# Optimization experiments

Hardware: AMD Instinct MI355X
Metric: run time of the kernel (lower is better)

The kernel has to match this reference:

```python
import jax, jax.numpy as jnp
import numpy as np

B, S, H = 2, 1024, 1024
NH, NKV, HD = 16, 4, 64
E, K, I = 8, 2, 3584
EPS = 1e-5
THETA = 1e6


def setup_inputs() -> dict:
    key = jax.random.key(0)
    ks = jax.random.split(key, 12)
    sc = 0.02
    return {
        "hidden_states": jax.random.normal(ks[0], (B, S, H), jnp.float32),
        "ln1_w": jnp.ones((H,), jnp.float32),
        "wq": jax.random.normal(ks[1], (H, NH * HD), jnp.float32) * sc,
        "wk": jax.random.normal(ks[2], (H, NKV * HD), jnp.float32) * sc,
        "wv": jax.random.normal(ks[3], (H, NKV * HD), jnp.float32) * sc,
        "wo": jax.random.normal(ks[4], (NH * HD, H), jnp.float32) * sc,
        "ln2_w": jnp.ones((H,), jnp.float32),
        "router_w": jax.random.normal(ks[5], (H, E), jnp.float32) * sc,
        "w_gate": jax.random.normal(ks[6], (E, H, I), jnp.float32) * sc,
        "w_up": jax.random.normal(ks[7], (E, H, I), jnp.float32) * sc,
        "w_down": jax.random.normal(ks[8], (E, I, H), jnp.float32) * sc,
    }


def _rmsnorm(x, w):
    xf = x.astype(jnp.float32)
    return (xf * jax.lax.rsqrt(jnp.mean(xf * xf, axis=-1, keepdims=True) + EPS)).astype(x.dtype) * w


def _rope_cos_sin():
    inv_freq = 1.0 / (THETA ** (jnp.arange(0, HD, 2, dtype=jnp.float32) / HD))
    ang = jnp.arange(S, dtype=jnp.float32)[:, None] * inv_freq[None, :]  # [S, HD//2]
    emb = jnp.concatenate([ang, ang], axis=-1)  # [S, HD]
    return jnp.cos(emb)[None, :, None, :], jnp.sin(emb)[None, :, None, :]


def _rotate_half(x):
    return jnp.concatenate([-x[..., HD // 2:], x[..., : HD // 2]], axis=-1)


def _attention(x, wq, wk, wv, wo):
    q = (x @ wq).reshape(B, S, NH, HD)
    k = (x @ wk).reshape(B, S, NKV, HD)
    v = (x @ wv).reshape(B, S, NKV, HD)
    cos, sin = _rope_cos_sin()
    q = q * cos + _rotate_half(q) * sin
    k = k * cos + _rotate_half(k) * sin
    rep = NH // NKV
    k = jnp.repeat(k, rep, axis=2)  # [B,S,NH,HD]
    v = jnp.repeat(v, rep, axis=2)
    scores = jnp.einsum("bqhd,bkhd->bhqk", q, k) / jnp.sqrt(jnp.float32(HD))
    causal = jnp.tril(jnp.ones((S, S), bool))
    scores = jnp.where(causal[None, None], scores, jnp.float32(-1e9))
    probs = jax.nn.softmax(scores, axis=-1)
    out = jnp.einsum("bhqk,bkhd->bqhd", probs, v).reshape(B, S, NH * HD)
    return out @ wo


def _moe(x, router_w, w_gate, w_up, w_down):
    t = x.reshape(B * S, H)  # [T,H]
    logits = t @ router_w  # [T,E]
    probs = jax.nn.softmax(logits.astype(jnp.float32), axis=-1)
    top_v, top_i = jax.lax.top_k(probs, K)
    top_v = top_v / jnp.sum(top_v, axis=-1, keepdims=True)  # normalize_top_k_affinities
    # dense combine weights [T,E]
    dense_w = jnp.sum(jax.nn.one_hot(top_i, E, dtype=t.dtype) * top_v[..., None], axis=1)
    out = jnp.zeros_like(t)
    for e in range(E):  # small fixed expert loop (E=8)
        g = jax.nn.silu(t @ w_gate[e]) * (t @ w_up[e])
        out = out + dense_w[:, e:e + 1] * (g @ w_down[e])
    return out.reshape(B, S, H)


def reference(hidden_states, ln1_w, wq, wk, wv, wo, ln2_w, router_w, w_gate, w_up, w_down):
    residual = hidden_states
    h = _rmsnorm(hidden_states, ln1_w)
    h = residual + _attention(h, wq, wk, wv, wo)
    residual = h
    h2 = _rmsnorm(h, ln2_w)
    h = residual + _moe(h2, router_w, w_gate, w_up, w_down)
    return h
```

## Files before the change

### kernel.cpp

```cpp
#include <hip/hip_runtime.h>
#include <hip/hip_bf16.h>
#include <math.h>

#define B_ 2
#define S_ 1024
#define H_ 1024
#define NH_ 16
#define NKV_ 4
#define HD_ 64
#define E_ 8
#define I_ 3584
#define T_ (B_*S_)

#define BM 64
#define BN 64
#define BK 32
#define MBM 128
#define MBK 64

typedef __bf16 bf16x8 __attribute__((ext_vector_type(8)));
typedef float f32x4 __attribute__((ext_vector_type(4)));

__device__ __forceinline__ __bf16 bf_hi(float f) { return (__bf16)f; }
__device__ __forceinline__ __bf16 bf_lo(float f, __bf16 h) { return (__bf16)(f - (float)h); }

__device__ __forceinline__ int swz(int row, int col) {
    return (row * 64 + col * 2) ^ (((row >> 3) & 7) << 4);
}
__device__ __forceinline__ int swz128(int row, int col) {
    return (row * 128 + col * 2) ^ ((row & 7) << 4);
}

__global__ __launch_bounds__(256) void cvt_bf16_kernel(
    const float* __restrict__ src, __bf16* __restrict__ dst, int n8)
{
    int idx = blockIdx.x * 256 + threadIdx.x;
    if (idx >= n8) return;
    const float4* s = (const float4*)src + (size_t)idx * 2;
    float4 a = s[0], b = s[1];
    bf16x8 v;
    v[0] = (__bf16)a.x; v[1] = (__bf16)a.y; v[2] = (__bf16)a.z; v[3] = (__bf16)a.w;
    v[4] = (__bf16)b.x; v[5] = (__bf16)b.y; v[6] = (__bf16)b.z; v[7] = (__bf16)b.w;
    ((bf16x8*)dst)[idx] = v;
}

__global__ __launch_bounds__(256) void transpose_cvt_kernel(
    const float* __restrict__ src, __bf16* __restrict__ dst, int M, int N)
{
    int e = blockIdx.z;
    src += (size_t)e * M * N;
    dst += (size_t)e * M * N;
    int n0 = blockIdx.x * 64, m0 = blockIdx.y * 64;
    __shared__ __bf16 Ts[64][72];
    int tid = threadIdx.x;
#pragma unroll
    for (int i = 0; i < 16; i++) {
        int row = i * 4 + (tid >> 6);
        int col = tid & 63;
        Ts[row][col] = (__bf16)src[(size_t)(m0 + row) * N + n0 + col];
    }
    __syncthreads();
#pragma unroll
    for (int j = 0; j < 2; j++) {
        int n = (tid >> 3) + j * 32;
        int k8 = (tid & 7) * 8;
        bf16x8 v;
#pragma unroll
        for (int ii = 0; ii < 8; ii++) v[ii] = Ts[k8 + ii][n];
        *(bf16x8*)(dst + (size_t)(n0 + n) * M + m0 + k8) = v;
    }
}

__global__ __launch_bounds__(256) void rmsnorm_kernel(
    const float* __restrict__ x, const float* __restrict__ w, float* __restrict__ out)
{
    int row = blockIdx.x;
    int tid = threadIdx.x;
    const float* xr = x + (size_t)row * H_;
    float vals[4];
    float ss = 0.f;
#pragma unroll
    for (int i = 0; i < 4; i++) {
        vals[i] = xr[tid + 256 * i];
        ss += vals[i] * vals[i];
    }
#pragma unroll
    for (int off = 32; off; off >>= 1) ss += __shfl_xor(ss, off);
    __shared__ float red[4];
    int wid = tid >> 6;
    if ((tid & 63) == 0) red[wid] = ss;
    __syncthreads();
    float tot = red[0] + red[1] + red[2] + red[3];
    float scale = rsqrtf(tot * (1.0f / H_) + 1e-5f);
#pragma unroll
    for (int i = 0; i < 4; i++)
        out[(size_t)row * H_ + tid + 256 * i] = vals[i] * scale * w[tid + 256 * i];
}

__global__ __launch_bounds__(256) void gemm_bf16(
    const float* __restrict__ A, const float* __restrict__ Bm,
    float* __restrict__ C, const float* __restrict__ res,
    int M, int N, int Kd)
{
    __shared__ __bf16 As[BM * BK];
    __shared__ __bf16 Bs[BN * BK];
    char* Asb = (char*)As;
    char* Bsb = (char*)Bs;
    int tid = threadIdx.x;
    int lane = tid & 63, wid = tid >> 6;
    int wm = wid >> 1, wn = wid & 1;
    int m0 = blockIdx.y * BM, n0 = blockIdx.x * BN;
    f32x4 acc[2][2] = {};
    int ar = tid >> 2, ac = (tid & 3) * 8;
    int bk = tid >> 3, bc = (tid & 7) * 8;
    for (int kt = 0; kt < Kd; kt += BK) {
        const float* ag = A + (size_t)(m0 + ar) * Kd + kt + ac;
        bf16x8 av;
#pragma unroll
        for (int i = 0; i < 8; i++) av[i] = (__bf16)ag[i];
        *(bf16x8*)(Asb + swz(ar, ac)) = av;
        const float* bg = Bm + (size_t)(kt + bk) * N + n0 + bc;
#pragma unroll
        for (int i = 0; i < 8; i++)
            *(__bf16*)(Bsb + swz(bc + i, bk)) = (__bf16)bg[i];
        __syncthreads();
        int r = lane & 15, k8 = (lane >> 4) * 8;
        bf16x8 af[2], bfr[2];
#pragma unroll
        for (int m = 0; m < 2; m++) af[m] = *(const bf16x8*)(Asb + swz(wm * 32 + m * 16 + r, k8));
#pragma unroll
        for (int n = 0; n < 2; n++) bfr[n] = *(const bf16x8*)(Bsb + swz(wn * 32 + n * 16 + r, k8));
#pragma unroll
        for (int m = 0; m < 2; m++)
#pragma unroll
            for (int n = 0; n < 2; n++)
                acc[m][n] = __builtin_amdgcn_mfma_f32_16x16x32_bf16(af[m], bfr[n], acc[m][n], 0, 0, 0);
        __syncthreads();
    }
    int cl = lane & 15, rb = (lane >> 4) * 4;
#pragma unroll
    for (int m = 0; m < 2; m++)
#pragma unroll
        for (int n = 0; n < 2; n++)
#pragma unroll
            for (int j = 0; j < 4; j++) {
                int row = m0 + wm * 32 + m * 16 + rb + j;
                int col = n0 + wn * 32 + n * 16 + cl;
                size_t o = (size_t)row * N + col;
                float v = acc[m][n][j];
                if (res) v += res[o];
                C[o] = v;
            }
}

__global__ void rope_kernel(float* __restrict__ x, int heads, int total)
{
    int idx = blockIdx.x * blockDim.x + threadIdx.x;
    if (idx >= total) return;
    int j = idx & 31;
    int th = idx >> 5;
    int h = th % heads;
    int t = th / heads;
    int s = t & (S_ - 1);
    float inv = powf(1e6f, -(float)j / 32.0f);
    float ang = (float)s * inv;
    float c = cosf(ang), sn = sinf(ang);
    size_t base = (size_t)t * heads * HD_ + (size_t)h * HD_;
    float x1 = x[base + j], x2 = x[base + 32 + j];
    x[base + j] = x1 * c - x2 * sn;
    x[base + 32 + j] = x2 * c + x1 * sn;
}

#define LP 72
__global__ __launch_bounds__(256) void flash_kernel(
    const float* __restrict__ q, const float* __restrict__ k,
    const float* __restrict__ v, float* __restrict__ o)
{
    __shared__ __bf16 Ks [64][LP];
    __shared__ __bf16 Ksl[64][LP];
    __shared__ __bf16 Vt [64][LP];
    __shared__ __bf16 Vtl[64][LP];
    __shared__ __bf16 Pl [4][16][LP];
    __shared__ __bf16 Pll[4][16][LP];

    int tid = threadIdx.x;
    int lane = tid & 63, wid = tid >> 6;
    int qr = lane & 15, quad = lane >> 4;
    int qt = (S_ / 16 - 1) - blockIdx.x;
    int kvh = blockIdx.y, b = blockIdx.z;
    int h = kvh * 4 + wid;
    int s0 = qt * 16;

    const float* qg = q + ((size_t)(b * S_ + s0 + qr) * NH_ + h) * HD_ + quad * 8;
    bf16x8 qf[2], qlo[2];
#pragma unroll
    for (int ks = 0; ks < 2; ks++)
#pragma unroll
        for (int i = 0; i < 8; i++) {
            float f = qg[ks * 32 + i] * 0.125f;
            __bf16 hh = bf_hi(f);
            qf[ks][i] = hh;
            qlo[ks][i] = bf_lo(f, hh);
        }

    float m_run[4], l_run[4];
    f32x4 o_acc[4] = {};
#pragma unroll
    for (int j = 0; j < 4; j++) { m_run[j] = -1e30f; l_run[j] = 0.f; }

    int skey = tid >> 2, shd0 = (tid & 3) * 16;
    int vhd = tid & 63, vkey0 = (tid >> 6) * 16;

    for (int kt = 0; kt <= s0 + 15; kt += 64) {
        __syncthreads();
        {
            const float* kg = k + ((size_t)(b * S_ + kt + skey) * NKV_ + kvh) * HD_ + shd0;
#pragma unroll
            for (int i = 0; i < 16; i++) {
                float f = kg[i];
                __bf16 hh = bf_hi(f);
                Ks [skey][shd0 + i] = hh;
                Ksl[skey][shd0 + i] = bf_lo(f, hh);
            }
        }
        {
            const float* vg = v + ((size_t)(b * S_ + kt + vkey0) * NKV_ + kvh) * HD_ + vhd;
#pragma unroll
            for (int i = 0; i < 16; i++) {
                float val = vg[(size_t)i * (NKV_ * HD_)];
                __bf16 hh = bf_hi(val);
                Vt [vhd][vkey0 + i] = hh;
                Vtl[vhd][vkey0 + i] = bf_lo(val, hh);
            }
        }
        __syncthreads();

        f32x4 sc4[4];
#pragma unroll
        for (int sub = 0; sub < 4; sub++) {
            int krow = sub * 16 + qr;
            bf16x8 kh0 = *(const bf16x8*)&Ks [krow][quad * 8];
            bf16x8 kh1 = *(const bf16x8*)&Ks [krow][32 + quad * 8];
            bf16x8 kl0 = *(const bf16x8*)&Ksl[krow][quad * 8];
            bf16x8 kl1 = *(const bf16x8*)&Ksl[krow][32 + quad * 8];
            f32x4 z = {};
            z = __builtin_amdgcn_mfma_f32_16x16x32_bf16(qf[0],  kh0, z, 0, 0, 0);
            z = __builtin_amdgcn_mfma_f32_16x16x32_bf16(qf[1],  kh1, z, 0, 0, 0);
            z = __builtin_amdgcn_mfma_f32_16x16x32_bf16(qlo[0], kh0, z, 0, 0, 0);
            z = __builtin_amdgcn_mfma_f32_16x16x32_bf16(qlo[1], kh1, z, 0, 0, 0);
            z = __builtin_amdgcn_mfma_f32_16x16x32_bf16(qf[0],  kl0, z, 0, 0, 0);
            z = __builtin_amdgcn_mfma_f32_16x16x32_bf16(qf[1],  kl1, z, 0, 0, 0);
            sc4[sub] = z;
        }
        if (kt + 63 > s0) {
#pragma unroll
            for (int sub = 0; sub < 4; sub++)
#pragma unroll
                for (int j = 0; j < 4; j++) {
                    int key = kt + sub * 16 + qr;
                    int row = s0 + quad * 4 + j;
                    if (key > row) sc4[sub][j] = -1e30f;
                }
        }
#pragma unroll
        for (int j = 0; j < 4; j++) {
            float mx = fmaxf(fmaxf(sc4[0][j], sc4[1][j]), fmaxf(sc4[2][j], sc4[3][j]));
#pragma unroll
            for (int off = 1; off < 16; off <<= 1) mx = fmaxf(mx, __shfl_xor(mx, off));
            float mn = fmaxf(m_run[j], mx);
            float scale = __expf(m_run[j] - mn);
            m_run[j] = mn;
            float rs = 0.f;
#pragma unroll
            for (int sub = 0; sub < 4; sub++) {
                float pe = __expf(sc4[sub][j] - mn);
                sc4[sub][j] = pe;
                rs += pe;
            }
#pragma unroll
            for (int off = 1; off < 16; off <<= 1) rs += __shfl_xor(rs, off);
            l_run[j] = l_run[j] * scale + rs;
#pragma unroll
            for (int sub = 0; sub < 4; sub++) o_acc[sub][j] *= scale;
        }
#pragma unroll
        for (int sub = 0; sub < 4; sub++)
#pragma unroll
            for (int j = 0; j < 4; j++) {
                float pe = sc4[sub][j];
                __bf16 hh = bf_hi(pe);
                Pl [wid][quad * 4 + j][sub * 16 + qr] = hh;
                Pll[wid][quad * 4 + j][sub * 16 + qr] = bf_lo(pe, hh);
            }
        __syncthreads();
        bf16x8 ph0 = *(const bf16x8*)&Pl [wid][qr][quad * 8];
        bf16x8 ph1 = *(const bf16x8*)&Pl [wid][qr][32 + quad * 8];
        bf16x8 pl0 = *(const bf16x8*)&Pll[wid][qr][quad * 8];
        bf16x8 pl1 = *(const bf16x8*)&Pll[wid][qr][32 + quad * 8];
#pragma unroll
        for (int sub = 0; sub < 4; sub++) {
            int vrow = sub * 16 + qr;
            bf16x8 vh0 = *(const bf16x8*)&Vt [vrow][quad * 8];
            bf16x8 vh1 = *(const bf16x8*)&Vt [vrow][32 + quad * 8];
            bf16x8 vl0 = *(const bf16x8*)&Vtl[vrow][quad * 8];
            bf16x8 vl1 = *(const bf16x8*)&Vtl[vrow][32 + quad * 8];
            o_acc[sub] = __builtin_amdgcn_mfma_f32_16x16x32_bf16(ph0, vh0, o_acc[sub], 0, 0, 0);
            o_acc[sub] = __builtin_amdgcn_mfma_f32_16x16x32_bf16(ph1, vh1, o_acc[sub], 0, 0, 0);
            o_acc[sub] = __builtin_amdgcn_mfma_f32_16x16x32_bf16(ph0, vl0, o_acc[sub], 0, 0, 0);
            o_acc[sub] = __builtin_amdgcn_mfma_f32_16x16x32_bf16(ph1, vl1, o_acc[sub], 0, 0, 0);
            o_acc[sub] = __builtin_amdgcn_mfma_f32_16x16x32_bf16(pl0, vh0, o_acc[sub], 0, 0, 0);
            o_acc[sub] = __builtin_amdgcn_mfma_f32_16x16x32_bf16(pl1, vh1, o_acc[sub], 0, 0, 0);
        }
    }
#pragma unroll
    for (int j = 0; j < 4; j++) {
        float inv = 1.f / l_run[j];
        int row = s0 + quad * 4 + j;
#pragma unroll
        for (int sub = 0; sub < 4; sub++)
            o[((size_t)(b * S_ + row) * NH_ + h) * HD_ + sub * 16 + qr] = o_acc[sub][j] * inv;
    }
}

__global__ __launch_bounds__(256) void router_kernel(
    const float* __restrict__ xn, const float* __restrict__ rw,
    int* __restrict__ top_i, float* __restrict__ top_w)
{
    int wid = threadIdx.x >> 6, lane = threadIdx.x & 63;
    int t = blockIdx.x * 4 + wid;
    const float* xr = xn + (size_t)t * H_;
    float acc[E_] = {};
    for (int c = 0; c < H_ / 64; c++) {
        float xd = xr[c * 64 + lane];
        const float* wrow = rw + (size_t)(c * 64 + lane) * E_;
#pragma unroll
        for (int e = 0; e < E_; e++) acc[e] += xd * wrow[e];
    }
#pragma unroll
    for (int e = 0; e < E_; e++) {
        float r = acc[e];
#pragma unroll
        for (int off = 32; off; off >>= 1) r += __shfl_xor(r, off);
        acc[e] = r;
    }
    if (lane == 0) {
        float mx = acc[0];
        for (int e = 1; e < E_; e++) mx = fmaxf(mx, acc[e]);
        float p[E_], sum = 0.f;
        for (int e = 0; e < E_; e++) { p[e] = __expf(acc[e] - mx); sum += p[e]; }
        float inv_s = 1.f / sum;
        for (int e = 0; e < E_; e++) p[e] *= inv_s;
        int i0 = 0;
        for (int e = 1; e < E_; e++) if (p[e] > p[i0]) i0 = e;
        int i1 = (i0 == 0) ? 1 : 0;
        for (int e = 0; e < E_; e++) if (e != i0 && p[e] > p[i1]) i1 = e;
        float v0 = p[i0], v1 = p[i1], inv = 1.f / (v0 + v1);
        top_i[t * 2] = i0; top_i[t * 2 + 1] = i1;
        top_w[t * 2] = v0 * inv; top_w[t * 2 + 1] = v1 * inv;
    }
}

__global__ void assign_kernel(
    const int* __restrict__ top_i, const float* __restrict__ top_w,
    int* __restrict__ tlist, int* __restrict__ pair_pos,
    int* __restrict__ counts, int* __restrict__ offsets)
{
    __shared__ int cnt[E_], off[E_], fill[E_];
    int tid = threadIdx.x;
    if (tid < E_) { cnt[tid] = 0; fill[tid] = 0; }
    __syncthreads();
    for (int t = tid; t < T_; t += 256) {
        atomicAdd(&cnt[top_i[t * 2]], 1);
        atomicAdd(&cnt[top_i[t * 2 + 1]], 1);
    }
    __syncthreads();
    if (tid == 0) {
        int o = 0;
        for (int e = 0; e < E_; e++) { off[e] = o; o += cnt[e]; }
    }
    __syncthreads();
    for (int t = tid; t < T_; t += 256) {
        for (int j = 0; j < 2; j++) {
            int e = top_i[t * 2 + j];
            int pos = off[e] + atomicAdd(&fill[e], 1);
            tlist[pos] = t;
            pair_pos[t * 2 + j] = pos;
        }
    }
    __syncthreads();
    if (tid < E_) { counts[tid] = cnt[tid]; offsets[tid] = off[tid]; }
}

__global__ __launch_bounds__(256) void moe_gemm_gateup(
    const __bf16* __restrict__ Xb, const __bf16* __restrict__ WgT, const __bf16* __restrict__ WuT,
    __bf16* __restrict__ act, const int* __restrict__ tlist,
    const int* __restrict__ counts, const int* __restrict__ offsets)
{
    int e = blockIdx.z;
    int cnt = counts[e], off = offsets[e];
    int m0 = blockIdx.y * MBM;
    if (m0 >= cnt) return;
    int n0 = blockIdx.x * BN;
    const __bf16* Bg = WgT + (size_t)e * H_ * I_;
    const __bf16* Bu = WuT + (size_t)e * H_ * I_;
    __shared__ __bf16 As[MBM * MBK];
    __shared__ __bf16 Gs[BN * MBK];
    __shared__ __bf16 Us[BN * MBK];
    __shared__ int rowidx[MBM];
    char* Asb = (char*)As;
    char* Gsb = (char*)Gs;
    char* Usb = (char*)Us;
    int tid = threadIdx.x;
    if (tid < MBM) {
        int rl = m0 + tid;
        rowidx[tid] = tlist[off + ((rl < cnt) ? rl : 0)];
    }
    __syncthreads();
    int lane = tid & 63, wid = tid >> 6;
    f32x4 accg[2][4] = {}, accu[2][4] = {};
    int ar = tid >> 1, ac = (tid & 1) * 32;
    int bn = tid >> 2, bc = (tid & 3) * 16;
    const __bf16* abase = Xb + (size_t)rowidx[ar] * H_;
    for (int kt = 0; kt < H_; kt += MBK) {
#pragma unroll
        for (int g = 0; g < 4; g++)
            *(bf16x8*)(Asb + swz128(ar, ac + g * 8)) =
                *(const bf16x8*)(abase + kt + ac + g * 8);
        const __bf16* gr = Bg + (size_t)(n0 + bn) * H_ + kt + bc;
        const __bf16* ur = Bu + (size_t)(n0 + bn) * H_ + kt + bc;
#pragma unroll
        for (int g = 0; g < 2; g++) {
            *(bf16x8*)(Gsb + swz128(bn, bc + g * 8)) = *(const bf16x8*)(gr + g * 8);
            *(bf16x8*)(Usb + swz128(bn, bc + g * 8)) = *(const bf16x8*)(ur + g * 8);
        }
        __syncthreads();
        int r = lane & 15, q8 = (lane >> 4) * 8;
#pragma unroll
        for (int kk = 0; kk < 2; kk++) {
            bf16x8 af[2], gf[4], uf[4];
#pragma unroll
            for (int m = 0; m < 2; m++)
                af[m] = *(const bf16x8*)(Asb + swz128(wid * 32 + m * 16 + r, kk * 32 + q8));
#pragma unroll
            for (int n = 0; n < 4; n++) {
                gf[n] = *(const bf16x8*)(Gsb + swz128(n * 16 + r, kk * 32 + q8));
                uf[n] = *(const bf16x8*)(Usb + swz128(n * 16 + r, kk * 32 + q8));
            }
#pragma unroll
            for (int m = 0; m < 2; m++)
#pragma unroll
                for (int n = 0; n < 4; n++) {
                    accg[m][n] = __builtin_amdgcn_mfma_f32_16x16x32_bf16(af[m], gf[n], accg[m][n], 0, 0, 0);
                    accu[m][n] = __builtin_amdgcn_mfma_f32_16x16x32_bf16(af[m], uf[n], accu[m][n], 0, 0, 0);
                }
        }
        __syncthreads();
    }
    int cl = lane & 15, rb = (lane >> 4) * 4;
#pragma unroll
    for (int m = 0; m < 2; m++)
#pragma unroll
        for (int n = 0; n < 4; n++)
#pragma unroll
            for (int j = 0; j < 4; j++) {
                int rl = m0 + wid * 32 + m * 16 + rb + j;
                if (rl >= cnt) continue;
                int col = n0 + n * 16 + cl;
                float g = accg[m][n][j], u = accu[m][n][j];
                float sig = 1.f / (1.f + __expf(-g));
                act[(size_t)(off + rl) * I_ + col] = (__bf16)(g * sig * u);
            }
}

__global__ __launch_bounds__(256) void moe_gemm_down(
    const __bf16* __restrict__ act, const __bf16* __restrict__ WdT,
    float* __restrict__ dout, const int* __restrict__ counts, const int* __restrict__ offsets)
{
    int e = blockIdx.z;
    int cnt = counts[e], off = offsets[e];
    int m0 = blockIdx.y * MBM;
    if (m0 >= cnt) return;
    int n0 = blockIdx.x * BN;
    const __bf16* Bw = WdT + (size_t)e * I_ * H_;
    __shared__ __bf16 As[MBM * MBK];
    __shared__ __bf16 Bs[BN * MBK];
    char* Asb = (char*)As;
    char* Bsb = (char*)Bs;
    int tid = threadIdx.x;
    int lane = tid & 63, wid = tid >> 6;
    f32x4 acc[2][4] = {};
    int ar = tid >> 1, ac = (tid & 1) * 32;
    int bn = tid >> 2, bc = (tid & 3) * 16;
    int arow = m0 + ar; if (arow >= cnt) arow = cnt - 1;
    const __bf16* abase = act + (size_t)(off + arow) * I_;
    for (int kt = 0; kt < I_; kt += MBK) {
#pragma unroll
        for (int g = 0; g < 4; g++)
            *(bf16x8*)(Asb + swz128(ar, ac + g * 8)) =
                *(const bf16x8*)(abase + kt + ac + g * 8);
        const __bf16* br = Bw + (size_t)(n0 + bn) * I_ + kt + bc;
#pragma unroll
        for (int g = 0; g < 2; g++)
            *(bf16x8*)(Bsb + swz128(bn, bc + g * 8)) = *(const bf16x8*)(br + g * 8);
        __syncthreads();
        int r = lane & 15, q8 = (lane >> 4) * 8;
#pragma unroll
        for (int kk = 0; kk < 2; kk++) {
            bf16x8 af[2], bfr[4];
#pragma unroll
            for (int m = 0; m < 2; m++)
                af[m] = *(const bf16x8*)(Asb + swz128(wid * 32 + m * 16 + r, kk * 32 + q8));
#pragma unroll
            for (int n = 0; n < 4; n++)
                bfr[n] = *(const bf16x8*)(Bsb + swz128(n * 16 + r, kk * 32 + q8));
#pragma unroll
            for (int m = 0; m < 2; m++)
#pragma unroll
                for (int n = 0; n < 4; n++)
                    acc[m][n] = __builtin_amdgcn_mfma_f32_16x16x32_bf16(af[m], bfr[n], acc[m][n], 0, 0, 0);
        }
        __syncthreads();
    }
    int cl = lane & 15, rb = (lane >> 4) * 4;
#pragma unroll
    for (int m = 0; m < 2; m++)
#pragma unroll
        for (int n = 0; n < 4; n++)
#pragma unroll
            for (int j = 0; j < 4; j++) {
                int rl = m0 + wid * 32 + m * 16 + rb + j;
                if (rl >= cnt) continue;
                int col = n0 + n * 16 + cl;
                dout[(size_t)(off + rl) * H_ + col] = acc[m][n][j];
            }
}

__global__ __launch_bounds__(256) void combine_kernel(
    const float* __restrict__ hres, const float* __restrict__ dout,
    const int* __restrict__ pair_pos, const float* __restrict__ top_w,
    float* __restrict__ out)
{
    int idx = blockIdx.x * 256 + threadIdx.x;
    int t = idx >> 10, d = idx & 1023;
    float v = hres[idx];
    int p0 = pair_pos[t * 2], p1 = pair_pos[t * 2 + 1];
    v += top_w[t * 2] * dout[(size_t)p0 * H_ + d]
       + top_w[t * 2 + 1] * dout[(size_t)p1 * H_ + d];
    out[idx] = v;
}

extern "C" void kernel_launch(void* const* d_in, const int* in_sizes, int n_in,
                              void* d_out, int out_size, void* d_ws, size_t ws_size,
                              hipStream_t stream) {
    const float* hidden = (const float*)d_in[0];
    const float* ln1 = (const float*)d_in[1];
    const float* wq = (const float*)d_in[2];
    const float* wk = (const float*)d_in[3];
    const float* wv = (const float*)d_in[4];
    const float* wo = (const float*)d_in[5];
    const float* ln2 = (const float*)d_in[6];
    const float* rw = (const float*)d_in[7];
    const float* wg = (const float*)d_in[8];
    const float* wu = (const float*)d_in[9];
    const float* wd = (const float*)d_in[10];
    float* out = (float*)d_out;

    char* ws = (char*)d_ws;
    size_t o = 0;
    auto alloc = [&](size_t bytes) -> void* {
        void* p = ws + o;
        o += (bytes + 255) & ~(size_t)255;
        return p;
    };
    float* xn   = (float*)alloc((size_t)T_ * H_ * 4);
    float* qb   = (float*)alloc((size_t)T_ * NH_ * HD_ * 4);
    float* kb   = (float*)alloc((size_t)T_ * NKV_ * HD_ * 4);
    float* vb   = (float*)alloc((size_t)T_ * NKV_ * HD_ * 4);
    float* attn = (float*)alloc((size_t)T_ * H_ * 4);
    float* hres = (float*)alloc((size_t)T_ * H_ * 4);
    int*   top_i    = (int*)alloc((size_t)T_ * 2 * 4);
    float* top_w    = (float*)alloc((size_t)T_ * 2 * 4);
    int*   pair_pos = (int*)alloc((size_t)T_ * 2 * 4);
    int*   tlist    = (int*)alloc((size_t)T_ * 2 * 4);
    int*   counts   = (int*)alloc(E_ * 4);
    int*   offsets  = (int*)alloc(E_ * 4);
    __bf16* actb  = (__bf16*)alloc((size_t)T_ * 2 * I_ * 2);
    float*  doutb = (float*)alloc((size_t)T_ * 2 * H_ * 4);
    __bf16* xnb = (__bf16*)alloc((size_t)T_ * H_ * 2);
    __bf16* wgt = (__bf16*)alloc((size_t)E_ * H_ * I_ * 2);
    __bf16* wut = (__bf16*)alloc((size_t)E_ * H_ * I_ * 2);
    __bf16* wdt = (__bf16*)alloc((size_t)E_ * I_ * H_ * 2);

    transpose_cvt_kernel<<<dim3(I_ / 64, H_ / 64, E_), 256, 0, stream>>>(wg, wgt, H_, I_);
    transpose_cvt_kernel<<<dim3(I_ / 64, H_ / 64, E_), 256, 0, stream>>>(wu, wut, H_, I_);
    transpose_cvt_kernel<<<dim3(H_ / 64, I_ / 64, E_), 256, 0, stream>>>(wd, wdt, I_, H_);

    rmsnorm_kernel<<<T_, 256, 0, stream>>>(hidden, ln1, xn);
    gemm_bf16<<<dim3((NH_ * HD_) / BN, T_ / BM), 256, 0, stream>>>(xn, wq, qb, nullptr, T_, NH_ * HD_, H_);
    gemm_bf16<<<dim3((NKV_ * HD_) / BN, T_ / BM), 256, 0, stream>>>(xn, wk, kb, nullptr, T_, NKV_ * HD_, H_);
    gemm_bf16<<<dim3((NKV_ * HD_) / BN, T_ / BM), 256, 0, stream>>>(xn, wv, vb, nullptr, T_, NKV_ * HD_, H_);
    {
        int tq = T_ * NH_ * 32, tk = T_ * NKV_ * 32;
        rope_kernel<<<(tq + 255) / 256, 256, 0, stream>>>(qb, NH_, tq);
        rope_kernel<<<(tk + 255) / 256, 256, 0, stream>>>(kb, NKV_, tk);
    }
    flash_kernel<<<dim3(S_ / 16, NKV_, B_), 256, 0, stream>>>(qb, kb, vb, attn);
    gemm_bf16<<<dim3(H_ / BN, T_ / BM), 256, 0, stream>>>(attn, wo, hres, hidden, T_, H_, H_);
    rmsnorm_kernel<<<T_, 256, 0, stream>>>(hres, ln2, xn);
    cvt_bf16_kernel<<<(T_ * H_ / 8 + 255) / 256, 256, 0, stream>>>(xn, xnb, T_ * H_ / 8);
    router_kernel<<<T_ / 4, 256, 0, stream>>>(xn, rw, top_i, top_w);
    assign_kernel<<<1, 256, 0, stream>>>(top_i, top_w, tlist, pair_pos, counts, offsets);
    moe_gemm_gateup<<<dim3(I_ / BN, T_ / MBM, E_), 256, 0, stream>>>(xnb, wgt, wut, actb, tlist, counts, offsets);
    moe_gemm_down<<<dim3(H_ / BN, T_ / MBM, E_), 256, 0, stream>>>(actb, wdt, doutb, counts, offsets);
    combine_kernel<<<(T_ * H_) / 256, 256, 0, stream>>>(hres, doutb, pair_pos, top_w, out);
}
```

Before: 524.4 us.

## Prefetch next K-tile into registers in MoE GEMMs and shrink down-proj M tile

Both MoE GEMM kernels now load the next K-tile from global memory into registers while MFMAs run on the current shared-memory tile, so load latency can overlap with compute. The down-projection also drops its M tile from 128 to 64 rows, doubling the grid so more workgroups are available for the roughly 512 assigned tokens per expert. This costs extra registers for the prefetch buffers and reuses each weight tile across fewer rows in the down GEMM.

```diff
diff --git a/kernel.cpp b/kernel.cpp
--- a/kernel.cpp
+++ b/kernel.cpp
@@ -16,6 +16,7 @@
 #define BN 64
 #define BK 32
 #define MBM 128
+#define DBM 64
 #define MBK 64
 
 typedef __bf16 bf16x8 __attribute__((ext_vector_type(8)));
@@ -420,20 +421,36 @@
     f32x4 accg[2][4] = {}, accu[2][4] = {};
     int ar = tid >> 1, ac = (tid & 1) * 32;
     int bn = tid >> 2, bc = (tid & 3) * 16;
-    const __bf16* abase = Xb + (size_t)rowidx[ar] * H_;
+    const __bf16* abase = Xb + (size_t)rowidx[ar] * H_ + ac;
+    const __bf16* gbase = Bg + (size_t)(n0 + bn) * H_ + bc;
+    const __bf16* ubase = Bu + (size_t)(n0 + bn) * H_ + bc;
+    bf16x8 pa[4], pg[2], pu[2];
+#pragma unroll
+    for (int g = 0; g < 4; g++) pa[g] = *(const bf16x8*)(abase + g * 8);
+#pragma unroll
+    for (int g = 0; g < 2; g++) {
+        pg[g] = *(const bf16x8*)(gbase + g * 8);
+        pu[g] = *(const bf16x8*)(ubase + g * 8);
+    }
     for (int kt = 0; kt < H_; kt += MBK) {
 #pragma unroll
-        for (int g = 0; g < 4; g++)
-            *(bf16x8*)(Asb + swz128(ar, ac + g * 8)) =
-                *(const bf16x8*)(abase + kt + ac + g * 8);
-        const __bf16* gr = Bg + (size_t)(n0 + bn) * H_ + kt + bc;
-        const __bf16* ur = Bu + (size_t)(n0 + bn) * H_ + kt + bc;
+        for (int g = 0; g < 4; g++) *(bf16x8*)(Asb + swz128(ar, ac + g * 8)) = pa[g];
 #pragma unroll
         for (int g = 0; g < 2; g++) {
-            *(bf16x8*)(Gsb + swz128(bn, bc + g * 8)) = *(const bf16x8*)(gr + g * 8);
-            *(bf16x8*)(Usb + swz128(bn, bc + g * 8)) = *(const bf16x8*)(ur + g * 8);
-        }
-        __syncthreads();
+            *(bf16x8*)(Gsb + swz128(bn, bc + g * 8)) = pg[g];
+            *(bf16x8*)(Usb + swz128(bn, bc + g * 8)) = pu[g];
+        }
+        __syncthreads();
+        int kn = kt + MBK;
+        if (kn < H_) {
+#pragma unroll
+            for (int g = 0; g < 4; g++) pa[g] = *(const bf16x8*)(abase + kn + g * 8);
+#pragma unroll
+            for (int g = 0; g < 2; g++) {
+                pg[g] = *(const bf16x8*)(gbase + kn + g * 8);
+                pu[g] = *(const bf16x8*)(ubase + kn + g * 8);
+            }
+        }
         int r = lane & 15, q8 = (lane >> 4) * 8;
 #pragma unroll
         for (int kk = 0; kk < 2; kk++) {
@@ -478,61 +495,67 @@
 {
     int e = blockIdx.z;
     int cnt = counts[e], off = offsets[e];
-    int m0 = blockIdx.y * MBM;
+    int m0 = blockIdx.y * DBM;
     if (m0 >= cnt) return;
     int n0 = blockIdx.x * BN;
     const __bf16* Bw = WdT + (size_t)e * I_ * H_;
-    __shared__ __bf16 As[MBM * MBK];
+    __shared__ __bf16 As[DBM * MBK];
     __shared__ __bf16 Bs[BN * MBK];
     char* Asb = (char*)As;
     char* Bsb = (char*)Bs;
     int tid = threadIdx.x;
     int lane = tid & 63, wid = tid >> 6;
-    f32x4 acc[2][4] = {};
-    int ar = tid >> 1, ac = (tid & 1) * 32;
+    f32x4 acc[4] = {};
+    int ar = tid >> 2, ac = (tid & 3) * 16;
     int bn = tid >> 2, bc = (tid & 3) * 16;
     int arow = m0 + ar; if (arow >= cnt) arow = cnt - 1;
-    const __bf16* abase = act + (size_t)(off + arow) * I_;
+    const __bf16* abase = act + (size_t)(off + arow) * I_ + ac;
+    const __bf16* bbase = Bw + (size_t)(n0 + bn) * I_ + bc;
+    bf16x8 pa[2], pb[2];
+#pragma unroll
+    for (int g = 0; g < 2; g++) {
+        pa[g] = *(const bf16x8*)(abase + g * 8);
+        pb[g] = *(const bf16x8*)(bbase + g * 8);
+    }
     for (int kt = 0; kt < I_; kt += MBK) {
 #pragma unroll
-        for (int g = 0; g < 4; g++)
-            *(bf16x8*)(Asb + swz128(ar, ac + g * 8)) =
-                *(const bf16x8*)(abase + kt + ac + g * 8);
-        const __bf16* br = Bw + (size_t)(n0 + bn) * I_ + kt + bc;
-#pragma unroll
-        for (int g = 0; g < 2; g++)
-            *(bf16x8*)(Bsb + swz128(bn, bc + g * 8)) = *(const bf16x8*)(br + g * 8);
-        __syncthreads();
+        for (int g = 0; g < 2; g++) {
+            *(bf16x8*)(Asb + swz128(ar, ac + g * 8)) = pa[g];
+            *(bf16x8*)(Bsb + swz128(bn, bc + g * 8)) = pb[g];
+        }
+        __syncthreads();
+        int kn = kt + MBK;
+        if (kn < I_) {
+#pragma unroll
+            for (int g = 0; g < 2; g++) {
+                pa[g] = *(const bf16x8*)(abase + kn + g * 8);
+                pb[g] = *(const bf16x8*)(bbase + kn + g * 8);
+            }
+        }
         int r = lane & 15, q8 = (lane >> 4) * 8;
 #pragma unroll
         for (int kk = 0; kk < 2; kk++) {
-            bf16x8 af[2], bfr[4];
-#pragma unroll
-            for (int m = 0; m < 2; m++)
-                af[m] = *(const bf16x8*)(Asb + swz128(wid * 32 + m * 16 + r, kk * 32 + q8));
+            bf16x8 af = *(const bf16x8*)(Asb + swz128(wid * 16 + r, kk * 32 + q8));
+            bf16x8 bfr[4];
 #pragma unroll
             for (int n = 0; n < 4; n++)
                 bfr[n] = *(const bf16x8*)(Bsb + swz128(n * 16 + r, kk * 32 + q8));
 #pragma unroll
-            for (int m = 0; m < 2; m++)
-#pragma unroll
-                for (int n = 0; n < 4; n++)
-                    acc[m][n] = __builtin_amdgcn_mfma_f32_16x16x32_bf16(af[m], bfr[n], acc[m][n], 0, 0, 0);
+            for (int n = 0; n < 4; n++)
+                acc[n] = __builtin_amdgcn_mfma_f32_16x16x32_bf16(af, bfr[n], acc[n], 0, 0, 0);
         }
         __syncthreads();
     }
     int cl = lane & 15, rb = (lane >> 4) * 4;
 #pragma unroll
-    for (int m = 0; m < 2; m++)
-#pragma unroll
-        for (int n = 0; n < 4; n++)
-#pragma unroll
-            for (int j = 0; j < 4; j++) {
-                int rl = m0 + wid * 32 + m * 16 + rb + j;
-                if (rl >= cnt) continue;
-                int col = n0 + n * 16 + cl;
-                dout[(size_t)(off + rl) * H_ + col] = acc[m][n][j];
-            }
+    for (int n = 0; n < 4; n++)
+#pragma unroll
+        for (int j = 0; j < 4; j++) {
+            int rl = m0 + wid * 16 + rb + j;
+            if (rl >= cnt) continue;
+            int col = n0 + n * 16 + cl;
+            dout[(size_t)(off + rl) * H_ + col] = acc[n][j];
+        }
 }
 
 __global__ __launch_bounds__(256) void combine_kernel(
@@ -611,6 +634,6 @@
     router_kernel<<<T_ / 4, 256, 0, stream>>>(xn, rw, top_i, top_w);
     assign_kernel<<<1, 256, 0, stream>>>(top_i, top_w, tlist, pair_pos, counts, offsets);
     moe_gemm_gateup<<<dim3(I_ / BN, T_ / MBM, E_), 256, 0, stream>>>(xnb, wgt, wut, actb, tlist, counts, offsets);
-    moe_gemm_down<<<dim3(H_ / BN, T_ / MBM, E_), 256, 0, stream>>>(actb, wdt, doutb, counts, offsets);
+    moe_gemm_down<<<dim3(H_ / BN, T_ / DBM, E_), 256, 0, stream>>>(actb, wdt, doutb, counts, offsets);
     combine_kernel<<<(T_ * H_) / 256, 256, 0, stream>>>(hres, doutb, pair_pos, top_w, out);
 }
```

Measured after the change: 500.0 us. 1.05x faster.

## Double-buffer MoE weight tiles and load activation fragments directly from global

Applied to the files above, without the earlier changes.

Both MoE GEMM kernels now halve the K tile, keep the weight tiles in double-buffered shared memory with register prefetch of the next tile, and read the A (activation) MFMA fragments straight from global memory instead of staging them in LDS. This removes one barrier per iteration and the A-tile LDS traffic, aiming to overlap global weight loads with MFMA work. In exchange each iteration issues uncoalesced per-lane global loads for A, and there are twice as many iterations with less MFMA work between barriers.

```diff
diff --git a/kernel.cpp b/kernel.cpp
--- a/kernel.cpp
+++ b/kernel.cpp
@@ -16,7 +16,7 @@
 #define BN 64
 #define BK 32
 #define MBM 128
-#define MBK 64
+#define MBK 32
 
 typedef __bf16 bf16x8 __attribute__((ext_vector_type(8)));
 typedef float f32x4 __attribute__((ext_vector_type(4)));
@@ -27,8 +27,8 @@
 __device__ __forceinline__ int swz(int row, int col) {
     return (row * 64 + col * 2) ^ (((row >> 3) & 7) << 4);
 }
-__device__ __forceinline__ int swz128(int row, int col) {
-    return (row * 128 + col * 2) ^ ((row & 7) << 4);
+__device__ __forceinline__ int swz64(int row, int col) {
+    return (row * 64 + col * 2) ^ (((row >> 1) & 3) << 4);
 }
 
 __global__ __launch_bounds__(256) void cvt_bf16_kernel(
@@ -403,13 +403,9 @@
     int n0 = blockIdx.x * BN;
     const __bf16* Bg = WgT + (size_t)e * H_ * I_;
     const __bf16* Bu = WuT + (size_t)e * H_ * I_;
-    __shared__ __bf16 As[MBM * MBK];
-    __shared__ __bf16 Gs[BN * MBK];
-    __shared__ __bf16 Us[BN * MBK];
+    __shared__ __bf16 Gs[2][BN * MBK];
+    __shared__ __bf16 Us[2][BN * MBK];
     __shared__ int rowidx[MBM];
-    char* Asb = (char*)As;
-    char* Gsb = (char*)Gs;
-    char* Usb = (char*)Us;
     int tid = threadIdx.x;
     if (tid < MBM) {
         int rl = m0 + tid;
@@ -417,44 +413,48 @@
     }
     __syncthreads();
     int lane = tid & 63, wid = tid >> 6;
+    int r = lane & 15, q8 = (lane >> 4) * 8;
+    const __bf16* arow0 = Xb + (size_t)rowidx[wid * 32 + r] * H_;
+    const __bf16* arow1 = Xb + (size_t)rowidx[wid * 32 + 16 + r] * H_;
+    int bn = tid >> 2, bc = (tid & 3) * 8;
+    const __bf16* gbase = Bg + (size_t)(n0 + bn) * H_ + bc;
+    const __bf16* ubase = Bu + (size_t)(n0 + bn) * H_ + bc;
+    *(bf16x8*)((char*)Gs[0] + swz64(bn, bc)) = *(const bf16x8*)(gbase);
+    *(bf16x8*)((char*)Us[0] + swz64(bn, bc)) = *(const bf16x8*)(ubase);
+    bf16x8 pg = *(const bf16x8*)(gbase + MBK);
+    bf16x8 pu = *(const bf16x8*)(ubase + MBK);
     f32x4 accg[2][4] = {}, accu[2][4] = {};
-    int ar = tid >> 1, ac = (tid & 1) * 32;
-    int bn = tid >> 2, bc = (tid & 3) * 16;
-    const __bf16* abase = Xb + (size_t)rowidx[ar] * H_;
+    int cur = 0;
     for (int kt = 0; kt < H_; kt += MBK) {
-#pragma unroll
-        for (int g = 0; g < 4; g++)
-            *(bf16x8*)(Asb + swz128(ar, ac + g * 8)) =
-                *(const bf16x8*)(abase + kt + ac + g * 8);
-        const __bf16* gr = Bg + (size_t)(n0 + bn) * H_ + kt + bc;
-        const __bf16* ur = Bu + (size_t)(n0 + bn) * H_ + kt + bc;
-#pragma unroll
-        for (int g = 0; g < 2; g++) {
-            *(bf16x8*)(Gsb + swz128(bn, bc + g * 8)) = *(const bf16x8*)(gr + g * 8);
-            *(bf16x8*)(Usb + swz128(bn, bc + g * 8)) = *(const bf16x8*)(ur + g * 8);
-        }
         __syncthreads();
-        int r = lane & 15, q8 = (lane >> 4) * 8;
-#pragma unroll
-        for (int kk = 0; kk < 2; kk++) {
-            bf16x8 af[2], gf[4], uf[4];
-#pragma unroll
-            for (int m = 0; m < 2; m++)
-                af[m] = *(const bf16x8*)(Asb + swz128(wid * 32 + m * 16 + r, kk * 32 + q8));
-#pragma unroll
-            for (int n = 0; n < 4; n++) {
-                gf[n] = *(const bf16x8*)(Gsb + swz128(n * 16 + r, kk * 32 + q8));
-                uf[n] = *(const bf16x8*)(Usb + swz128(n * 16 + r, kk * 32 + q8));
-            }
-#pragma unroll
-            for (int m = 0; m < 2; m++)
-#pragma unroll
-                for (int n = 0; n < 4; n++) {
-                    accg[m][n] = __builtin_amdgcn_mfma_f32_16x16x32_bf16(af[m], gf[n], accg[m][n], 0, 0, 0);
-                    accu[m][n] = __builtin_amdgcn_mfma_f32_16x16x32_bf16(af[m], uf[n], accu[m][n], 0, 0, 0);
-                }
-        }
-        __syncthreads();
+        char* Gsb = (char*)Gs[cur];
+        char* Usb = (char*)Us[cur];
+        bf16x8 af0 = *(const bf16x8*)(arow0 + kt + q8);
+        bf16x8 af1 = *(const bf16x8*)(arow1 + kt + q8);
+        bf16x8 gf[4], uf[4];
+#pragma unroll
+        for (int n = 0; n < 4; n++) {
+            gf[n] = *(const bf16x8*)(Gsb + swz64(n * 16 + r, q8));
+            uf[n] = *(const bf16x8*)(Usb + swz64(n * 16 + r, q8));
+        }
+#pragma unroll
+        for (int n = 0; n < 4; n++) {
+            accg[0][n] = __builtin_amdgcn_mfma_f32_16x16x32_bf16(af0, gf[n], accg[0][n], 0, 0, 0);
+            accg[1][n] = __builtin_amdgcn_mfma_f32_16x16x32_bf16(af1, gf[n], accg[1][n], 0, 0, 0);
+            accu[0][n] = __builtin_amdgcn_mfma_f32_16x16x32_bf16(af0, uf[n], accu[0][n], 0, 0, 0);
+            accu[1][n] = __builtin_amdgcn_mfma_f32_16x16x32_bf16(af1, uf[n], accu[1][n], 0, 0, 0);
+        }
+        int kn = kt + MBK;
+        if (kn < H_) {
+            *(bf16x8*)((char*)Gs[cur ^ 1] + swz64(bn, bc)) = pg;
+            *(bf16x8*)((char*)Us[cur ^ 1] + swz64(bn, bc)) = pu;
+            int k2 = kn + MBK;
+            if (k2 < H_) {
+                pg = *(const bf16x8*)(gbase + k2);
+                pu = *(const bf16x8*)(ubase + k2);
+            }
+            cur ^= 1;
+        }
     }
     int cl = lane & 15, rb = (lane >> 4) * 4;
 #pragma unroll
@@ -482,44 +482,41 @@
     if (m0 >= cnt) return;
     int n0 = blockIdx.x * BN;
     const __bf16* Bw = WdT + (size_t)e * I_ * H_;
-    __shared__ __bf16 As[MBM * MBK];
-    __shared__ __bf16 Bs[BN * MBK];
-    char* Asb = (char*)As;
-    char* Bsb = (char*)Bs;
+    __shared__ __bf16 Bs[2][BN * MBK];
     int tid = threadIdx.x;
     int lane = tid & 63, wid = tid >> 6;
+    int r = lane & 15, q8 = (lane >> 4) * 8;
+    int row0 = m0 + wid * 32 + r;      if (row0 >= cnt) row0 = cnt - 1;
+    int row1 = m0 + wid * 32 + 16 + r; if (row1 >= cnt) row1 = cnt - 1;
+    const __bf16* arow0 = act + (size_t)(off + row0) * I_;
+    const __bf16* arow1 = act + (size_t)(off + row1) * I_;
+    int bn = tid >> 2, bc = (tid & 3) * 8;
+    const __bf16* bbase = Bw + (size_t)(n0 + bn) * I_ + bc;
+    *(bf16x8*)((char*)Bs[0] + swz64(bn, bc)) = *(const bf16x8*)(bbase);
+    bf16x8 pb = *(const bf16x8*)(bbase + MBK);
     f32x4 acc[2][4] = {};
-    int ar = tid >> 1, ac = (tid & 1) * 32;
-    int bn = tid >> 2, bc = (tid & 3) * 16;
-    int arow = m0 + ar; if (arow >= cnt) arow = cnt - 1;
-    const __bf16* abase = act + (size_t)(off + arow) * I_;
+    int cur = 0;
     for (int kt = 0; kt < I_; kt += MBK) {
-#pragma unroll
-        for (int g = 0; g < 4; g++)
-            *(bf16x8*)(Asb + swz128(ar, ac + g * 8)) =
-                *(const bf16x8*)(abase + kt + ac + g * 8);
-        const __bf16* br = Bw + (size_t)(n0 + bn) * I_ + kt + bc;
-#pragma unroll
-        for (int g = 0; g < 2; g++)
-            *(bf16x8*)(Bsb + swz128(bn, bc + g * 8)) = *(const bf16x8*)(br + g * 8);
         __syncthreads();
-        int r = lane & 15, q8 = (lane >> 4) * 8;
-#pragma unroll
-        for (int kk = 0; kk < 2; kk++) {
-            bf16x8 af[2], bfr[4];
-#pragma unroll
-            for (int m = 0; m < 2; m++)
-                af[m] = *(const bf16x8*)(Asb + swz128(wid * 32 + m * 16 + r, kk * 32 + q8));
-#pragma unroll
-            for (int n = 0; n < 4; n++)
-                bfr[n] = *(const bf16x8*)(Bsb + swz128(n * 16 + r, kk * 32 + q8));
-#pragma unroll
-            for (int m = 0; m < 2; m++)
-#pragma unroll
-                for (int n = 0; n < 4; n++)
-                    acc[m][n] = __builtin_amdgcn_mfma_f32_16x16x32_bf16(af[m], bfr[n], acc[m][n], 0, 0, 0);
-        }
-        __syncthreads();
+        char* Bsb = (char*)Bs[cur];
+        bf16x8 af0 = *(const bf16x8*)(arow0 + kt + q8);
+        bf16x8 af1 = *(const bf16x8*)(arow1 + kt + q8);
+        bf16x8 bfr[4];
+#pragma unroll
+        for (int n = 0; n < 4; n++)
+            bfr[n] = *(const bf16x8*)(Bsb + swz64(n * 16 + r, q8));
+#pragma unroll
+        for (int n = 0; n < 4; n++) {
+            acc[0][n] = __builtin_amdgcn_mfma_f32_16x16x32_bf16(af0, bfr[n], acc[0][n], 0, 0, 0);
+            acc[1][n] = __builtin_amdgcn_mfma_f32_16x16x32_bf16(af1, bfr[n], acc[1][n], 0, 0, 0);
+        }
+        int kn = kt + MBK;
+        if (kn < I_) {
+            *(bf16x8*)((char*)Bs[cur ^ 1] + swz64(bn, bc)) = pb;
+            int k2 = kn + MBK;
+            if (k2 < I_) pb = *(const bf16x8*)(bbase + k2);
+            cur ^= 1;
+        }
     }
     int cl = lane & 15, rb = (lane >> 4) * 4;
 #pragma unroll
```

Measured after the change: 529.0 us. No clear change (+0.9%).
